# Kernel optimization log

Measured on AMD Instinct MI355X. Metric: run time of the kernel, lower is better.

Reference implementation:

```python
import jax, jax.numpy as jnp
import numpy as np

B, N, E, H = 1, 4096, 1024, 16
D = E // H

def setup_inputs() -> dict:
    key = jax.random.key(0)
    k1, k2, k3 = jax.random.split(key, 3)
    s = 1.0 / np.sqrt(E)
    return {
        "x": jax.random.normal(k1, (B, N, E), dtype=jnp.float32),
        "w_qkv": jax.random.normal(k2, (3 * E, E), dtype=jnp.float32) * s,
        "b_qkv": jnp.zeros((3 * E,), dtype=jnp.float32),
        "w_proj": jax.random.normal(k3, (E, E), dtype=jnp.float32) * s,
        "b_proj": jnp.zeros((E,), dtype=jnp.float32),
    }

def reference(x, w_qkv, b_qkv, w_proj, b_proj):
    Bx, Nx, Ex = x.shape
    scale = (Ex // H) ** -0.5
    # torch Linear: x @ W^T + b
    qkv = jnp.einsum('bne,fe->bnf', x, w_qkv) + b_qkv  # [B,N,3E]
    q, k, v = jnp.split(qkv, 3, axis=-1)
    def to_heads(t):
        return t.reshape(Bx, Nx, H, Ex // H).transpose(0, 2, 1, 3)  # b h n d
    q, k, v = to_heads(q), to_heads(k), to_heads(v)
    dots = jnp.einsum('bhnd,bhmd->bhnm', q, k) * scale  # full NxN scores
    attn = jax.nn.softmax(dots, axis=-1)  # dropout=0 (eval)
    out = jnp.einsum('bhnm,bhmd->bhnd', attn, v)
    out = out.transpose(0, 2, 1, 3).reshape(Bx, Nx, Ex)
    return jnp.einsum('bne,fe->bnf', out, w_proj) + b_proj
```

## Files before the change

### kernel.cpp

```cpp
#include <hip/hip_runtime.h>

#define N_TOK 4096
#define E_DIM 1024
#define NH    16
#define HD    64

typedef __bf16 bf16x8 __attribute__((ext_vector_type(8)));
typedef __bf16 bf16x4 __attribute__((ext_vector_type(4)));
typedef float  f32x4  __attribute__((ext_vector_type(4)));
typedef float  f32x16 __attribute__((ext_vector_type(16)));

#define GLOAD16(gsrc, ldst) __builtin_amdgcn_global_load_lds( \
    (const __attribute__((address_space(1))) void*)(gsrc),    \
    (__attribute__((address_space(3))) void*)(ldst), 16, 0, 0)

__device__ __forceinline__ f32x16 zero16() {
    f32x16 z;
#pragma unroll
    for (int i = 0; i < 16; ++i) z[i] = 0.f;
    return z;
}

__device__ __forceinline__ unsigned pk2(float a, float b) {
    union { __bf16 h[2]; unsigned u; } t;
    t.h[0] = (__bf16)a; t.h[1] = (__bf16)b;
    return t.u;
}

__device__ __forceinline__ void load16(const __bf16* __restrict__ p, bf16x8& lo, bf16x8& hi) {
    lo = *(const bf16x8*)p;
    hi = *(const bf16x8*)(p + 8);
}

__global__ __launch_bounds__(256) void conv_bf16(const float* __restrict__ src,
                                                 __bf16* __restrict__ dst, int n8) {
    const int i = blockIdx.x * 256 + threadIdx.x;
    if (i >= n8) return;
    const float4 a = ((const float4*)src)[i * 2];
    const float4 b = ((const float4*)src)[i * 2 + 1];
    ((bf16x8*)dst)[i] = bf16x8{(__bf16)a.x, (__bf16)a.y, (__bf16)a.z, (__bf16)a.w,
                               (__bf16)b.x, (__bf16)b.y, (__bf16)b.z, (__bf16)b.w};
}

__device__ __forceinline__ void gemm_core(const __bf16* __restrict__ A, const __bf16* __restrict__ B,
                                          const int K, const int rowBase, const int colBase,
                                          __bf16* As, __bf16* Bs, f32x4 (&acc)[4][4]) {
    const int tid = threadIdx.x, lane = tid & 63, wid = tid >> 6;
    const int wm = wid >> 1, wn = wid & 1;
    const int lr = lane & 15, lg = lane >> 4;
    const int lrow = lane >> 2, lcol = (lane & 3) * 8;

    const __bf16* aBase = A + (size_t)(rowBase + wid * 16 + lrow) * K + lcol;
    const __bf16* bBase = B + (size_t)(colBase + wid * 16 + lrow) * K + lcol;
    const size_t row64 = (size_t)64 * K;

    for (int kt = 0; kt < K; kt += 32) {
        __syncthreads();
        GLOAD16(aBase + kt,         As + wid * 512);
        GLOAD16(aBase + row64 + kt, As + 2048 + wid * 512);
        GLOAD16(bBase + kt,         Bs + wid * 512);
        GLOAD16(bBase + row64 + kt, Bs + 2048 + wid * 512);
        __syncthreads();

        bf16x8 af[4], bfr[4];
#pragma unroll
        for (int i = 0; i < 4; ++i) {
            af[i]  = *(const bf16x8*)&As[(wm * 64 + i * 16 + lr) * 32 + lg * 8];
            bfr[i] = *(const bf16x8*)&Bs[(wn * 64 + i * 16 + lr) * 32 + lg * 8];
        }
#pragma unroll
        for (int i = 0; i < 4; ++i)
#pragma unroll
            for (int j = 0; j < 4; ++j)
                acc[i][j] = __builtin_amdgcn_mfma_f32_16x16x32_bf16(af[i], bfr[j], acc[i][j], 0, 0, 0);
    }
}

#define QSCALE 0.180336879f

__global__ __launch_bounds__(256) void qkv_gemm(const __bf16* __restrict__ x,
                                                const __bf16* __restrict__ wqkv,
                                                const float* __restrict__ bqkv,
                                                __bf16* __restrict__ Qb,
                                                __bf16* __restrict__ Kb,
                                                __bf16* __restrict__ VtG) {
    __shared__ __bf16 As[128 * 32];
    __shared__ __bf16 Bs[128 * 32];
    f32x4 acc[4][4];
#pragma unroll
    for (int i = 0; i < 4; ++i)
#pragma unroll
        for (int j = 0; j < 4; ++j)
            acc[i][j] = f32x4{0.f, 0.f, 0.f, 0.f};

    const int lin = blockIdx.y * 32 + blockIdx.x;
    const int swz = (lin & 7) * 96 + (lin >> 3);
    const int tm = swz & 31, tn = swz >> 5;

    gemm_core(x, wqkv, E_DIM, tm * 128, tn * 128, As, Bs, acc);

    const int tid = threadIdx.x;
    const int lane = tid & 63, wid = tid >> 6;
    const int wm = wid >> 1, wn = wid & 1;
    const int lr = lane & 15, lg = lane >> 4;

#pragma unroll
    for (int ni = 0; ni < 4; ++ni) {
        const int f = tn * 128 + wn * 64 + ni * 16 + lr;
        const float bias = bqkv[f];
        const int which = f >> 10;
        const int hh = (f & 1023) >> 6;
        const int dd = f & 63;
        if (which == 2) {
            __bf16* dst = VtG + ((size_t)hh * HD + dd) * N_TOK;
#pragma unroll
            for (int mi = 0; mi < 4; ++mi) {
                const int n0 = tm * 128 + wm * 64 + mi * 16 + lg * 4;
                const int pos = (n0 & ~12) | ((n0 & 4) << 1) | ((n0 & 8) >> 1);
                bf16x4 v;
#pragma unroll
                for (int r = 0; r < 4; ++r) v[r] = (__bf16)(acc[mi][ni][r] + bias);
                *(bf16x4*)&dst[pos] = v;
            }
        } else {
            __bf16* dst = (which == 0) ? Qb : Kb;
            const float sc = (which == 0) ? QSCALE : 1.0f;
#pragma unroll
            for (int mi = 0; mi < 4; ++mi) {
#pragma unroll
                for (int r = 0; r < 4; ++r) {
                    const int n = tm * 128 + wm * 64 + mi * 16 + lg * 4 + r;
                    dst[((size_t)hh * N_TOK + n) * HD + dd] = (__bf16)((acc[mi][ni][r] + bias) * sc);
                }
            }
        }
    }
}

#define QBLK  256
#define KVB   128
#define NTILE (N_TOK / KVB)
#define KST   72
#define VST   136
#define BUFSZ (KVB * KST + HD * VST)

__global__ __launch_bounds__(512, 2) void flash_attn(const __bf16* __restrict__ Qb,
                                                     const __bf16* __restrict__ Kb,
                                                     const __bf16* __restrict__ Vt,
                                                     __bf16* __restrict__ Ob) {
    __shared__ __bf16 smem[2 * BUFSZ];

    const int tid = threadIdx.x, lane = tid & 63, wid = tid >> 6;
    const int lq = lane & 31, hi = lane >> 5;
    const int qg = wid >> 1, hw = wid & 1;

    const int lin = blockIdx.y * 16 + blockIdx.x;
    const int swz = (lin & 7) * 32 + (lin >> 3);
    const int qblk = swz & 15, h = swz >> 4;

    const __bf16* Qh = Qb + (size_t)h * N_TOK * HD;
    const __bf16* Kh = Kb + (size_t)h * N_TOK * HD;
    const __bf16* Vh = Vt + (size_t)h * HD * N_TOK;

    bf16x8 qf[2][4];
#pragma unroll
    for (int g = 0; g < 2; ++g) {
        const size_t qr = (size_t)qblk * QBLK + qg * 64 + g * 32 + lq;
#pragma unroll
        for (int sd = 0; sd < 4; ++sd)
            qf[g][sd] = *(const bf16x8*)&Qh[qr * HD + sd * 16 + hi * 8];
    }

    f32x16 o[2][2], lacc[2];
#pragma unroll
    for (int g = 0; g < 2; ++g) { o[g][0] = zero16(); o[g][1] = zero16(); lacc[g] = zero16(); }
    float m[2] = {-INFINITY, -INFINITY};

    const bf16x8 ones = bf16x8{(__bf16)1.f, (__bf16)1.f, (__bf16)1.f, (__bf16)1.f,
                               (__bf16)1.f, (__bf16)1.f, (__bf16)1.f, (__bf16)1.f};

    const int krow = tid >> 2, kseg = (tid & 3) * 16;
    const int vrow = tid >> 3, vseg = (tid & 7) * 16;
    const __bf16* kSrc = Kh + (size_t)krow * HD + kseg;
    const __bf16* vSrc = Vh + (size_t)vrow * N_TOK + vseg;

    bf16x8 kr0, kr1, vr0, vr1;
    load16(kSrc, kr0, kr1);
    load16(vSrc, vr0, vr1);
    {
        __bf16* Kw = smem;
        __bf16* Vw = smem + KVB * KST;
        *(bf16x8*)&Kw[krow * KST + kseg]     = kr0;
        *(bf16x8*)&Kw[krow * KST + kseg + 8] = kr1;
        *(bf16x8*)&Vw[vrow * VST + vseg]     = vr0;
        *(bf16x8*)&Vw[vrow * VST + vseg + 8] = vr1;
    }

    for (int t = 0; t < NTILE; ++t) {
        const int cur = t & 1;
        const __bf16* Kc = smem + cur * BUFSZ;
        const __bf16* Vc = Kc + KVB * KST;

        if (t + 1 < NTILE) {
            load16(kSrc + (size_t)(t + 1) * KVB * HD, kr0, kr1);
            load16(vSrc + (t + 1) * KVB, vr0, vr1);
        }
        __syncthreads();

        f32x16 s[2][2];
#pragma unroll
        for (int g = 0; g < 2; ++g) { s[g][0] = zero16(); s[g][1] = zero16(); }
        __builtin_amdgcn_s_setprio(1);
#pragma unroll
        for (int sd = 0; sd < 4; ++sd) {
            const bf16x8 kf0 = *(const bf16x8*)&Kc[(hw * 64 + lq) * KST + sd * 16 + hi * 8];
            const bf16x8 kf1 = *(const bf16x8*)&Kc[(hw * 64 + 32 + lq) * KST + sd * 16 + hi * 8];
            s[0][0] = __builtin_amdgcn_mfma_f32_32x32x16_bf16(kf0, qf[0][sd], s[0][0], 0, 0, 0);
            s[0][1] = __builtin_amdgcn_mfma_f32_32x32x16_bf16(kf1, qf[0][sd], s[0][1], 0, 0, 0);
            s[1][0] = __builtin_amdgcn_mfma_f32_32x32x16_bf16(kf0, qf[1][sd], s[1][0], 0, 0, 0);
            s[1][1] = __builtin_amdgcn_mfma_f32_32x32x16_bf16(kf1, qf[1][sd], s[1][1], 0, 0, 0);
        }
        __builtin_amdgcn_s_setprio(0);

        float mx[2];
#pragma unroll
        for (int g = 0; g < 2; ++g) {
            const float t0 = fmaxf(fmaxf(s[g][0][0],  s[g][0][1]),  fmaxf(s[g][0][2],  s[g][0][3]));
            const float t1 = fmaxf(fmaxf(s[g][0][4],  s[g][0][5]),  fmaxf(s[g][0][6],  s[g][0][7]));
            const float t2 = fmaxf(fmaxf(s[g][0][8],  s[g][0][9]),  fmaxf(s[g][0][10], s[g][0][11]));
            const float t3 = fmaxf(fmaxf(s[g][0][12], s[g][0][13]), fmaxf(s[g][0][14], s[g][0][15]));
            const float t4 = fmaxf(fmaxf(s[g][1][0],  s[g][1][1]),  fmaxf(s[g][1][2],  s[g][1][3]));
            const float t5 = fmaxf(fmaxf(s[g][1][4],  s[g][1][5]),  fmaxf(s[g][1][6],  s[g][1][7]));
            const float t6 = fmaxf(fmaxf(s[g][1][8],  s[g][1][9]),  fmaxf(s[g][1][10], s[g][1][11]));
            const float t7 = fmaxf(fmaxf(s[g][1][12], s[g][1][13]), fmaxf(s[g][1][14], s[g][1][15]));
            const float u0 = fmaxf(fmaxf(t0, t1), fmaxf(t2, t3));
            const float u1 = fmaxf(fmaxf(t4, t5), fmaxf(t6, t7));
            float a = fmaxf(u0, u1);
            mx[g] = fmaxf(a, __shfl_xor(a, 32));
        }

        if (!__all(mx[0] <= m[0] + 8.f && mx[1] <= m[1] + 8.f)) {
#pragma unroll
            for (int g = 0; g < 2; ++g) {
                const float mn = fmaxf(m[g], mx[g]);
                const float al = __builtin_amdgcn_exp2f(m[g] - mn);
                m[g] = mn;
#pragma unroll
                for (int r = 0; r < 16; ++r) { o[g][0][r] *= al; o[g][1][r] *= al; }
                lacc[g][0] *= al;
            }
        }

#pragma unroll
        for (int w = 0; w < 4; ++w) {
            const int rb = (w & 1) * 8;
            const int half = (w < 2) ? 0 : 1;
            bf16x8 pfv[2];
#pragma unroll
            for (int g = 0; g < 2; ++g) {
                union { unsigned u[4]; bf16x8 v; } pf;
                pf.u[0] = pk2(__builtin_amdgcn_exp2f(s[g][half][rb + 0] - m[g]),
                              __builtin_amdgcn_exp2f(s[g][half][rb + 1] - m[g]));
                pf.u[1] = pk2(__builtin_amdgcn_exp2f(s[g][half][rb + 2] - m[g]),
                              __builtin_amdgcn_exp2f(s[g][half][rb + 3] - m[g]));
                pf.u[2] = pk2(__builtin_amdgcn_exp2f(s[g][half][rb + 4] - m[g]),
                              __builtin_amdgcn_exp2f(s[g][half][rb + 5] - m[g]));
                pf.u[3] = pk2(__builtin_amdgcn_exp2f(s[g][half][rb + 6] - m[g]),
                              __builtin_amdgcn_exp2f(s[g][half][rb + 7] - m[g]));
                pfv[g] = pf.v;
            }

            const bf16x8 vf0 = *(const bf16x8*)&Vc[lq * VST + hw * 64 + w * 16 + hi * 8];
            const bf16x8 vf1 = *(const bf16x8*)&Vc[(32 + lq) * VST + hw * 64 + w * 16 + hi * 8];
            __builtin_amdgcn_s_setprio(1);
            o[0][0] = __builtin_amdgcn_mfma_f32_32x32x16_bf16(vf0, pfv[0], o[0][0], 0, 0, 0);
            o[0][1] = __builtin_amdgcn_mfma_f32_32x32x16_bf16(vf1, pfv[0], o[0][1], 0, 0, 0);
            o[1][0] = __builtin_amdgcn_mfma_f32_32x32x16_bf16(vf0, pfv[1], o[1][0], 0, 0, 0);
            o[1][1] = __builtin_amdgcn_mfma_f32_32x32x16_bf16(vf1, pfv[1], o[1][1], 0, 0, 0);
            lacc[0] = __builtin_amdgcn_mfma_f32_32x32x16_bf16(ones, pfv[0], lacc[0], 0, 0, 0);
            lacc[1] = __builtin_amdgcn_mfma_f32_32x32x16_bf16(ones, pfv[1], lacc[1], 0, 0, 0);
            __builtin_amdgcn_s_setprio(0);
        }

        if (t + 1 < NTILE) {
            __bf16* Kw = smem + (cur ^ 1) * BUFSZ;
            __bf16* Vw = Kw + KVB * KST;
            *(bf16x8*)&Kw[krow * KST + kseg]     = kr0;
            *(bf16x8*)&Kw[krow * KST + kseg + 8] = kr1;
            *(bf16x8*)&Vw[vrow * VST + vseg]     = vr0;
            *(bf16x8*)&Vw[vrow * VST + vseg + 8] = vr1;
        }
    }

    __syncthreads();
    float* scratch = (float*)smem;
    if (hw == 1) {
#pragma unroll
        for (int g = 0; g < 2; ++g) {
            float* po = scratch + (qg * 2 + g) * 2080;
#pragma unroll
            for (int r = 0; r < 16; ++r) {
                const int d0 = (r & 3) + 8 * (r >> 2) + 4 * hi;
                po[lq * 65 + d0]      = o[g][0][r];
                po[lq * 65 + 32 + d0] = o[g][1][r];
            }
            if (hi == 0) {
                float* plm = scratch + 16640 + (qg * 2 + g) * 64;
                plm[lq * 2] = lacc[g][0]; plm[lq * 2 + 1] = m[g];
            }
        }
    }
    __syncthreads();
    if (hw == 0) {
#pragma unroll
        for (int g = 0; g < 2; ++g) {
            float* po  = scratch + (qg * 2 + g) * 2080;
            float* plm = scratch + 16640 + (qg * 2 + g) * 64;
            const float l1 = plm[lq * 2], m1 = plm[lq * 2 + 1];
            const float M  = fmaxf(m[g], m1);
            const float a0 = __builtin_amdgcn_exp2f(m[g] - M);
            const float a1 = __builtin_amdgcn_exp2f(m1 - M);
            const float inv = 1.0f / (lacc[g][0] * a0 + l1 * a1);
            const size_t qr = (size_t)qblk * QBLK + qg * 64 + g * 32 + lq;
            __bf16* obase = &Ob[qr * E_DIM + h * HD];
#pragma unroll
            for (int grp = 0; grp < 4; ++grp) {
                bf16x4 v0, v1;
#pragma unroll
                for (int c = 0; c < 4; ++c) {
                    const int r = grp * 4 + c;
                    const int d0 = c + 8 * grp + 4 * hi;
                    v0[c] = (__bf16)((o[g][0][r] * a0 + po[lq * 65 + d0]      * a1) * inv);
                    v1[c] = (__bf16)((o[g][1][r] * a0 + po[lq * 65 + 32 + d0] * a1) * inv);
                }
                *(bf16x4*)&obase[grp * 8 + hi * 4]      = v0;
                *(bf16x4*)&obase[32 + grp * 8 + hi * 4] = v1;
            }
        }
    }
}

__global__ __launch_bounds__(256) void proj_gemm(const __bf16* __restrict__ Ob,
                                                 const __bf16* __restrict__ wp,
                                                 const float* __restrict__ bp,
                                                 float* __restrict__ out) {
    __shared__ __bf16 As[128 * 32];
    __shared__ __bf16 Bs[128 * 32];
    f32x4 acc[4][4];
#pragma unroll
    for (int i = 0; i < 4; ++i)
#pragma unroll
        for (int j = 0; j < 4; ++j)
            acc[i][j] = f32x4{0.f, 0.f, 0.f, 0.f};

    const int lin = blockIdx.y * 32 + blockIdx.x;
    const int swz = (lin & 7) * 32 + (lin >> 3);
    const int tm = swz & 31, tn = swz >> 5;

    gemm_core(Ob, wp, E_DIM, tm * 128, tn * 128, As, Bs, acc);

    const int tid = threadIdx.x;
    const int lane = tid & 63, wid = tid >> 6;
    const int wm = wid >> 1, wn = wid & 1;
    const int lr = lane & 15, lg = lane >> 4;

#pragma unroll
    for (int ni = 0; ni < 4; ++ni) {
        const int f = tn * 128 + wn * 64 + ni * 16 + lr;
        const float bias = bp[f];
#pragma unroll
        for (int mi = 0; mi < 4; ++mi) {
#pragma unroll
            for (int r = 0; r < 4; ++r) {
                const int n = tm * 128 + wm * 64 + mi * 16 + lg * 4 + r;
                out[(size_t)n * E_DIM + f] = acc[mi][ni][r] + bias;
            }
        }
    }
}

extern "C" void kernel_launch(void* const* d_in, const int* in_sizes, int n_in,
                              void* d_out, int out_size, void* d_ws, size_t ws_size,
                              hipStream_t stream) {
    const float* x     = (const float*)d_in[0];
    const float* wqkv  = (const float*)d_in[1];
    const float* bqkv  = (const float*)d_in[2];
    const float* wproj = (const float*)d_in[3];
    const float* bproj = (const float*)d_in[4];
    float* out = (float*)d_out;

    const size_t headElems = (size_t)NH * N_TOK * HD;
    __bf16* Qb   = (__bf16*)d_ws;
    __bf16* Kb   = Qb + headElems;
    __bf16* VtG  = Kb + headElems;
    __bf16* ObXb = VtG + headElems;
    __bf16* Wb   = ObXb + headElems;

    conv_bf16<<<(N_TOK * E_DIM / 8 + 255) / 256, 256, 0, stream>>>(x, ObXb, N_TOK * E_DIM / 8);
    conv_bf16<<<(3 * E_DIM * E_DIM / 8 + 255) / 256, 256, 0, stream>>>(wqkv, Wb, 3 * E_DIM * E_DIM / 8);

    qkv_gemm<<<dim3(N_TOK / 128, 3 * E_DIM / 128), 256, 0, stream>>>(ObXb, Wb, bqkv, Qb, Kb, VtG);

    conv_bf16<<<(E_DIM * E_DIM / 8 + 255) / 256, 256, 0, stream>>>(wproj, Wb, E_DIM * E_DIM / 8);

    flash_attn<<<dim3(N_TOK / QBLK, NH), 512, 0, stream>>>(Qb, Kb, VtG, ObXb);

    proj_gemm<<<dim3(N_TOK / 128, E_DIM / 128), 256, 0, stream>>>(ObXb, Wb, bproj, out);
}
```

Measured before the change: 166.7 us.

## Double GEMM K-tile to 64, merge input conversions, use fmax3 reductions

The shared GEMM core now stages a 64-wide K slice per iteration, with each wave loading four 16-byte chunks per operand, and runs two MFMA sub-steps between barriers. This halves the number of barrier and load-issue rounds in the QKV and projection GEMMs, at the cost of doubling their LDS tiles to 32 KB per block. The x and w_qkv fp32-to-bf16 conversions are merged into one launch to remove a kernel launch. The attention row-max reduction is rewritten as three-input max chains that can map to v_max3 instructions.

```diff
diff --git a/kernel.cpp b/kernel.cpp
--- a/kernel.cpp
+++ b/kernel.cpp
@@ -27,19 +27,34 @@
     return t.u;
 }
 
+__device__ __forceinline__ float fmax3(float a, float b, float c) {
+    return fmaxf(fmaxf(a, b), c);
+}
+
 __device__ __forceinline__ void load16(const __bf16* __restrict__ p, bf16x8& lo, bf16x8& hi) {
     lo = *(const bf16x8*)p;
     hi = *(const bf16x8*)(p + 8);
+}
+
+__device__ __forceinline__ void cvt8(const float* __restrict__ src, __bf16* __restrict__ dst, int i) {
+    const float4 a = ((const float4*)src)[i * 2];
+    const float4 b = ((const float4*)src)[i * 2 + 1];
+    ((bf16x8*)dst)[i] = bf16x8{(__bf16)a.x, (__bf16)a.y, (__bf16)a.z, (__bf16)a.w,
+                               (__bf16)b.x, (__bf16)b.y, (__bf16)b.z, (__bf16)b.w};
+}
+
+__global__ __launch_bounds__(256) void conv_pair(const float* __restrict__ s1, __bf16* __restrict__ d1, int n1,
+                                                 const float* __restrict__ s2, __bf16* __restrict__ d2, int n2) {
+    const int i = blockIdx.x * 256 + threadIdx.x;
+    if (i < n1)            cvt8(s1, d1, i);
+    else if (i < n1 + n2)  cvt8(s2, d2, i - n1);
 }
 
 __global__ __launch_bounds__(256) void conv_bf16(const float* __restrict__ src,
                                                  __bf16* __restrict__ dst, int n8) {
     const int i = blockIdx.x * 256 + threadIdx.x;
     if (i >= n8) return;
-    const float4 a = ((const float4*)src)[i * 2];
-    const float4 b = ((const float4*)src)[i * 2 + 1];
-    ((bf16x8*)dst)[i] = bf16x8{(__bf16)a.x, (__bf16)a.y, (__bf16)a.z, (__bf16)a.w,
-                               (__bf16)b.x, (__bf16)b.y, (__bf16)b.z, (__bf16)b.w};
+    cvt8(src, dst, i);
 }
 
 __device__ __forceinline__ void gemm_core(const __bf16* __restrict__ A, const __bf16* __restrict__ B,
@@ -48,31 +63,34 @@
     const int tid = threadIdx.x, lane = tid & 63, wid = tid >> 6;
     const int wm = wid >> 1, wn = wid & 1;
     const int lr = lane & 15, lg = lane >> 4;
-    const int lrow = lane >> 2, lcol = (lane & 3) * 8;
-
-    const __bf16* aBase = A + (size_t)(rowBase + wid * 16 + lrow) * K + lcol;
-    const __bf16* bBase = B + (size_t)(colBase + wid * 16 + lrow) * K + lcol;
-    const size_t row64 = (size_t)64 * K;
-
-    for (int kt = 0; kt < K; kt += 32) {
+    const int lrow = lane >> 3, lcol = (lane & 7) * 8;
+
+    const __bf16* aBase = A + (size_t)(rowBase + wid * 32 + lrow) * K + lcol;
+    const __bf16* bBase = B + (size_t)(colBase + wid * 32 + lrow) * K + lcol;
+
+    for (int kt = 0; kt < K; kt += 64) {
         __syncthreads();
-        GLOAD16(aBase + kt,         As + wid * 512);
-        GLOAD16(aBase + row64 + kt, As + 2048 + wid * 512);
-        GLOAD16(bBase + kt,         Bs + wid * 512);
-        GLOAD16(bBase + row64 + kt, Bs + 2048 + wid * 512);
+#pragma unroll
+        for (int c = 0; c < 4; ++c) {
+            GLOAD16(aBase + (size_t)c * 8 * K + kt, As + wid * 2048 + c * 512);
+            GLOAD16(bBase + (size_t)c * 8 * K + kt, Bs + wid * 2048 + c * 512);
+        }
         __syncthreads();
 
-        bf16x8 af[4], bfr[4];
-#pragma unroll
-        for (int i = 0; i < 4; ++i) {
-            af[i]  = *(const bf16x8*)&As[(wm * 64 + i * 16 + lr) * 32 + lg * 8];
-            bfr[i] = *(const bf16x8*)&Bs[(wn * 64 + i * 16 + lr) * 32 + lg * 8];
-        }
-#pragma unroll
-        for (int i = 0; i < 4; ++i)
-#pragma unroll
-            for (int j = 0; j < 4; ++j)
-                acc[i][j] = __builtin_amdgcn_mfma_f32_16x16x32_bf16(af[i], bfr[j], acc[i][j], 0, 0, 0);
+#pragma unroll
+        for (int kk = 0; kk < 2; ++kk) {
+            bf16x8 af[4], bfr[4];
+#pragma unroll
+            for (int i = 0; i < 4; ++i) {
+                af[i]  = *(const bf16x8*)&As[(wm * 64 + i * 16 + lr) * 64 + kk * 32 + lg * 8];
+                bfr[i] = *(const bf16x8*)&Bs[(wn * 64 + i * 16 + lr) * 64 + kk * 32 + lg * 8];
+            }
+#pragma unroll
+            for (int i = 0; i < 4; ++i)
+#pragma unroll
+                for (int j = 0; j < 4; ++j)
+                    acc[i][j] = __builtin_amdgcn_mfma_f32_16x16x32_bf16(af[i], bfr[j], acc[i][j], 0, 0, 0);
+        }
     }
 }
 
@@ -84,8 +102,8 @@
                                                 __bf16* __restrict__ Qb,
                                                 __bf16* __restrict__ Kb,
                                                 __bf16* __restrict__ VtG) {
-    __shared__ __bf16 As[128 * 32];
-    __shared__ __bf16 Bs[128 * 32];
+    __shared__ __bf16 As[128 * 64];
+    __shared__ __bf16 Bs[128 * 64];
     f32x4 acc[4][4];
 #pragma unroll
     for (int i = 0; i < 4; ++i)
@@ -225,17 +243,21 @@
         float mx[2];
 #pragma unroll
         for (int g = 0; g < 2; ++g) {
-            const float t0 = fmaxf(fmaxf(s[g][0][0],  s[g][0][1]),  fmaxf(s[g][0][2],  s[g][0][3]));
-            const float t1 = fmaxf(fmaxf(s[g][0][4],  s[g][0][5]),  fmaxf(s[g][0][6],  s[g][0][7]));
-            const float t2 = fmaxf(fmaxf(s[g][0][8],  s[g][0][9]),  fmaxf(s[g][0][10], s[g][0][11]));
-            const float t3 = fmaxf(fmaxf(s[g][0][12], s[g][0][13]), fmaxf(s[g][0][14], s[g][0][15]));
-            const float t4 = fmaxf(fmaxf(s[g][1][0],  s[g][1][1]),  fmaxf(s[g][1][2],  s[g][1][3]));
-            const float t5 = fmaxf(fmaxf(s[g][1][4],  s[g][1][5]),  fmaxf(s[g][1][6],  s[g][1][7]));
-            const float t6 = fmaxf(fmaxf(s[g][1][8],  s[g][1][9]),  fmaxf(s[g][1][10], s[g][1][11]));
-            const float t7 = fmaxf(fmaxf(s[g][1][12], s[g][1][13]), fmaxf(s[g][1][14], s[g][1][15]));
-            const float u0 = fmaxf(fmaxf(t0, t1), fmaxf(t2, t3));
-            const float u1 = fmaxf(fmaxf(t4, t5), fmaxf(t6, t7));
-            float a = fmaxf(u0, u1);
+            const float t0 = fmax3(s[g][0][0],  s[g][0][1],  s[g][0][2]);
+            const float t1 = fmax3(s[g][0][3],  s[g][0][4],  s[g][0][5]);
+            const float t2 = fmax3(s[g][0][6],  s[g][0][7],  s[g][0][8]);
+            const float t3 = fmax3(s[g][0][9],  s[g][0][10], s[g][0][11]);
+            const float t4 = fmax3(s[g][0][12], s[g][0][13], s[g][0][14]);
+            const float t5 = fmax3(s[g][1][0],  s[g][1][1],  s[g][1][2]);
+            const float t6 = fmax3(s[g][1][3],  s[g][1][4],  s[g][1][5]);
+            const float t7 = fmax3(s[g][1][6],  s[g][1][7],  s[g][1][8]);
+            const float t8 = fmax3(s[g][1][9],  s[g][1][10], s[g][1][11]);
+            const float t9 = fmax3(s[g][1][12], s[g][1][13], s[g][1][14]);
+            const float u0 = fmax3(t0, t1, s[g][0][15]);
+            const float u1 = fmax3(t2, t3, t4);
+            const float u2 = fmax3(t5, t6, s[g][1][15]);
+            const float u3 = fmax3(t7, t8, t9);
+            float a = fmaxf(fmax3(u0, u1, u2), u3);
             mx[g] = fmaxf(a, __shfl_xor(a, 32));
         }
 
@@ -344,8 +366,8 @@
                                                  const __bf16* __restrict__ wp,
                                                  const float* __restrict__ bp,
                                                  float* __restrict__ out) {
-    __shared__ __bf16 As[128 * 32];
-    __shared__ __bf16 Bs[128 * 32];
+    __shared__ __bf16 As[128 * 64];
+    __shared__ __bf16 Bs[128 * 64];
     f32x4 acc[4][4];
 #pragma unroll
     for (int i = 0; i < 4; ++i)
@@ -396,8 +418,9 @@
     __bf16* ObXb = VtG + headElems;
     __bf16* Wb   = ObXb + headElems;
 
-    conv_bf16<<<(N_TOK * E_DIM / 8 + 255) / 256, 256, 0, stream>>>(x, ObXb, N_TOK * E_DIM / 8);
-    conv_bf16<<<(3 * E_DIM * E_DIM / 8 + 255) / 256, 256, 0, stream>>>(wqkv, Wb, 3 * E_DIM * E_DIM / 8);
+    const int n1 = N_TOK * E_DIM / 8;
+    const int n2 = 3 * E_DIM * E_DIM / 8;
+    conv_pair<<<(n1 + n2 + 255) / 256, 256, 0, stream>>>(x, ObXb, n1, wqkv, Wb, n2);
 
     qkv_gemm<<<dim3(N_TOK / 128, 3 * E_DIM / 128), 256, 0, stream>>>(ObXb, Wb, bqkv, Qb, Kb, VtG);
 
```

Result: slower. 177.2 us (+6.3%).
